# Performance work log

Measured on AMD Instinct MI355X. Metric: run time of the kernel, lower is better.

Reference implementation:

```python
import jax, jax.numpy as jnp
import numpy as np

E, R, K, D, B = 100000, 1000, 200, 256, 65536  # entities, relations, bundle heads, emb dim, batch


def setup_inputs() -> dict:
    key = jax.random.key(0)
    ks = jax.random.split(key, 12)
    ent_emb = jax.random.normal(ks[0], (E, D), dtype=jnp.float32)
    ent_emb = ent_emb / jnp.linalg.norm(ent_emb, axis=1, keepdims=True)  # xavier + L2 row-normalize
    heads = jax.random.normal(ks[1], (K, D), dtype=jnp.float32)
    heads = heads / jnp.linalg.norm(heads, axis=1, keepdims=True)  # normalize_vvrel_embeddings
    bases = jax.random.normal(ks[2], (R, 2, D), dtype=jnp.float32)
    bases = bases / jnp.linalg.norm(bases, axis=2, keepdims=True)  # normalize_all_rows
    rel2head = jax.random.randint(ks[3], (R,), 0, K)              # r_id2_vrr[rel][0] -> head idx
    rel2mult = jnp.where(jax.random.bernoulli(ks[4], 0.5, (R,)), 1.0, -1.0).astype(jnp.float32)  # r_id2_vrr[rel][1]
    return {
        'pos_h': jax.random.randint(ks[5], (B,), 0, E),
        'pos_t': jax.random.randint(ks[6], (B,), 0, E),
        'pos_r': jax.random.randint(ks[7], (B,), 0, R),
        'neg_h': jax.random.randint(ks[8], (B,), 0, E),
        'neg_t': jax.random.randint(ks[9], (B,), 0, E),
        'neg_r': jax.random.randint(ks[10], (B,), 0, R),
        'ent_emb': ent_emb, 'heads': heads, 'bases': bases,
        'rel2head': rel2head, 'rel2mult': rel2mult,
    }


def _transint_scores(pos_h, pos_t, pos_r, neg_h, neg_t, ent_emb, heads, bases, rel2head, rel2mult):
    # vvrel_embedding_func: head embedding scaled by +-1 multiplier
    r_e = heads[rel2head[pos_r]] * rel2mult[pos_r][:, None]           # [B, D]
    pos_sub = ent_emb[pos_h] + r_e - ent_emb[pos_t]                    # [B, D]
    neg_sub = ent_emb[neg_h] + r_e - ent_emb[neg_t]                    # [B, D] (note: uses pos_r_e, as in source)
    sub = jnp.concatenate([pos_sub, neg_sub], axis=0)                  # [2B, D]
    A = bases[jnp.concatenate([pos_r, pos_r], axis=0)]                 # [2B, 2, D] per-sample basis (comb_mats gather)
    # ATA and closed-form 2x2 inverse (module's `inverse`)
    ATA = jnp.einsum('bkd,bld->bkl', A, A)                             # [2B, 2, 2]
    a, b = ATA[:, 0, 0], ATA[:, 0, 1]
    c, d = ATA[:, 1, 0], ATA[:, 1, 1]
    det = a * d - b * c
    safe_det = jnp.where(det != 0, det, 1.0)
    inv_reg = jnp.stack([jnp.stack([d, -b], -1), jnp.stack([-c, a], -1)], -2) / safe_det[:, None, None]
    inv_fb = jnp.eye(2, dtype=ATA.dtype)[None] / a[:, None, None]      # fallback when det == 0
    ATA_inv = jnp.where((det != 0)[:, None, None], inv_reg, inv_fb)    # [2B, 2, 2]
    # P @ sub with P = I - A^T (A A^T)^{-1} A, applied without materializing P
    Asub = jnp.einsum('bkd,bd->bk', A, sub)                            # [2B, 2]
    proj = sub - jnp.einsum('bkd,bk->bd', A, jnp.einsum('bkl,bl->bk', ATA_inv, Asub))
    score = jnp.sum(proj ** 2, axis=1)                                 # L1_flag = False -> squared L2
    nb = pos_h.shape[0]
    return score[:nb], score[nb:]


def reference(pos_h, pos_t, pos_r, neg_h, neg_t, neg_r, ent_emb, heads, bases, rel2head, rel2mult):
    return _transint_scores(pos_h, pos_t, pos_r, neg_h, neg_t, ent_emb, heads, bases, rel2head, rel2mult)
```

## Files before the change

kernel.cpp:

```cpp
#include <hip/hip_runtime.h>

#define D 256
#define D4 (D/4)

__device__ inline float dot4(const float4 u, const float4 v) {
    return u.x*v.x + u.y*v.y + u.z*v.z + u.w*v.w;
}

__device__ inline float wsum(float v) {
    #pragma unroll
    for (int off = 32; off > 0; off >>= 1)
        v += __shfl_xor(v, off, 64);
    return v;
}

__global__ __launch_bounds__(256) void transint_pre(
    const float* __restrict__ heads,
    const float* __restrict__ bases,
    const int*   __restrict__ rel2head,
    const float* __restrict__ rel2mult,
    float*       __restrict__ re_buf,
    float*       __restrict__ par_buf,
    int R)
{
    const int wave = (blockIdx.x * blockDim.x + threadIdx.x) >> 6;
    const int lane = threadIdx.x & 63;
    if (wave >= R) return;
    const int r = wave;

    const int hd = rel2head[r];
    const float mult = rel2mult[r];
    const float4* hrow = (const float4*)(heads + (size_t)hd * D);
    const float4* arow = (const float4*)(bases + (size_t)r * 2 * D);

    float4 a0 = arow[lane];
    float4 a1 = arow[D4 + lane];
    float4 re = hrow[lane];
    re.x *= mult; re.y *= mult; re.z *= mult; re.w *= mult;
    ((float4*)(re_buf + (size_t)r * D))[lane] = re;

    float aa = wsum(dot4(a0, a0));
    float ab = wsum(dot4(a0, a1));
    float dd = wsum(dot4(a1, a1));

    float det = aa * dd - ab * ab;
    float m00, m01, m11;
    if (det != 0.0f) {
        float inv = 1.0f / det;
        m00 = dd * inv; m01 = -ab * inv; m11 = aa * inv;
    } else {
        float inv = 1.0f / aa;
        m00 = inv; m01 = 0.0f; m11 = inv;
    }
    if (lane == 0) {
        float* p = par_buf + (size_t)r * 8;
        p[0] = m00; p[1] = m01; p[2] = m11;
        p[3] = aa;  p[4] = ab;  p[5] = dd;
        p[6] = 0.0f; p[7] = 0.0f;
    }
}

__global__ __launch_bounds__(256) void transint_main(
    const int*   __restrict__ pos_h,
    const int*   __restrict__ pos_t,
    const int*   __restrict__ pos_r,
    const int*   __restrict__ neg_h,
    const int*   __restrict__ neg_t,
    const float* __restrict__ ent_emb,
    const float* __restrict__ bases,
    const float* __restrict__ re_buf,
    const float* __restrict__ par_buf,
    float*       __restrict__ out,
    int nB)
{
    const int wave = (blockIdx.x * blockDim.x + threadIdx.x) >> 6;
    const int lane = threadIdx.x & 63;
    const int g    = lane >> 4;
    const int gl   = lane & 15;
    const int b    = wave * 4 + g;
    if (b >= nB) return;

    const int r  = pos_r[b];
    const int ph = pos_h[b];
    const int pt = pos_t[b];
    const int nh = neg_h[b];
    const int nt = neg_t[b];

    const float4* e   = (const float4*)ent_emb;
    const float4* a0p = (const float4*)(bases + (size_t)r * 2 * D);
    const float4* a1p = a0p + D4;
    const float4* rep = (const float4*)(re_buf + (size_t)r * D);
    const float4* php = e + (size_t)ph * D4;
    const float4* ptp = e + (size_t)pt * D4;
    const float4* nhp = e + (size_t)nh * D4;
    const float4* ntp = e + (size_t)nt * D4;

    float p0 = 0.f, p1 = 0.f, n0 = 0.f, n1 = 0.f, ssp = 0.f, ssn = 0.f;

    #pragma unroll
    for (int c = 0; c < 4; ++c) {
        const int idx = gl + 16 * c;
        float4 a0 = a0p[idx];
        float4 a1 = a1p[idx];
        float4 re = rep[idx];
        float4 eh = php[idx];
        float4 et = ptp[idx];
        float4 xh = nhp[idx];
        float4 xt = ntp[idx];

        float4 ps, ns;
        ps.x = eh.x + re.x - et.x;  ns.x = xh.x + re.x - xt.x;
        ps.y = eh.y + re.y - et.y;  ns.y = xh.y + re.y - xt.y;
        ps.z = eh.z + re.z - et.z;  ns.z = xh.z + re.z - xt.z;
        ps.w = eh.w + re.w - et.w;  ns.w = xh.w + re.w - xt.w;

        p0  += dot4(a0, ps);
        p1  += dot4(a1, ps);
        n0  += dot4(a0, ns);
        n1  += dot4(a1, ns);
        ssp += dot4(ps, ps);
        ssn += dot4(ns, ns);
    }

    #pragma unroll
    for (int off = 8; off > 0; off >>= 1) {
        p0  += __shfl_xor(p0,  off, 64);
        p1  += __shfl_xor(p1,  off, 64);
        n0  += __shfl_xor(n0,  off, 64);
        n1  += __shfl_xor(n1,  off, 64);
        ssp += __shfl_xor(ssp, off, 64);
        ssn += __shfl_xor(ssn, off, 64);
    }

    const float* par = par_buf + (size_t)r * 8;
    const float m00 = par[0], m01 = par[1], m11 = par[2];
    const float aa  = par[3], ab  = par[4], dd  = par[5];

    float c0 = m00 * p0 + m01 * p1;
    float c1 = m01 * p0 + m11 * p1;
    float sp = ssp - 2.f * (p0 * c0 + p1 * c1)
             + (aa * c0 * c0 + 2.f * ab * c0 * c1 + dd * c1 * c1);

    float d0 = m00 * n0 + m01 * n1;
    float d1 = m01 * n0 + m11 * n1;
    float sn = ssn - 2.f * (n0 * d0 + n1 * d1)
             + (aa * d0 * d0 + 2.f * ab * d0 * d1 + dd * d1 * d1);

    if (gl == 0) {
        out[b]      = sp;
        out[nB + b] = sn;
    }
}

extern "C" void kernel_launch(void* const* d_in, const int* in_sizes, int n_in,
                              void* d_out, int out_size, void* d_ws, size_t ws_size,
                              hipStream_t stream) {
    const int*   pos_h    = (const int*)  d_in[0];
    const int*   pos_t    = (const int*)  d_in[1];
    const int*   pos_r    = (const int*)  d_in[2];
    const int*   neg_h    = (const int*)  d_in[3];
    const int*   neg_t    = (const int*)  d_in[4];
    const float* ent_emb  = (const float*)d_in[6];
    const float* heads    = (const float*)d_in[7];
    const float* bases    = (const float*)d_in[8];
    const int*   rel2head = (const int*)  d_in[9];
    const float* rel2mult = (const float*)d_in[10];
    float* out = (float*)d_out;

    const int nB = in_sizes[0];
    const int R  = in_sizes[9];

    float* re_buf  = (float*)d_ws;
    float* par_buf = re_buf + (size_t)R * D;

    {
        const int waves_per_block = 4;
        dim3 grid((R + waves_per_block - 1) / waves_per_block);
        transint_pre<<<grid, dim3(256), 0, stream>>>(
            heads, bases, rel2head, rel2mult, re_buf, par_buf, R);
    }

    {
        const int samples_per_block = 16;
        dim3 grid((nB + samples_per_block - 1) / samples_per_block);
        transint_main<<<grid, dim3(256), 0, stream>>>(
            pos_h, pos_t, pos_r, neg_h, neg_t,
            ent_emb, bases, re_buf, par_buf, out, nB);
    }
}
```

Before: 195.2 us.

## Convert entity table to fp16 per call and gather half-precision rows

Adds a pre-pass kernel that converts the whole entity embedding table to packed fp16 in workspace on every call. The main kernel then gathers half-width rows and unpacks them to fp32 for the projection math. The goal is to halve the bytes moved by the four random row gathers per sample. In exchange, each call pays a full-table read plus a half-size write, and the scores lose precision from fp16 rounding. The fp32 path is kept as a fallback when the workspace is too small.

```diff
diff --git a/kernel.cpp b/kernel.cpp
--- a/kernel.cpp
+++ b/kernel.cpp
@@ -2,6 +2,9 @@
 
 #define D 256
 #define D4 (D/4)
+#define D8 (D/8)
+
+typedef __fp16 f16x2 __attribute__((ext_vector_type(2)));
 
 __device__ inline float dot4(const float4 u, const float4 v) {
     return u.x*v.x + u.y*v.y + u.z*v.z + u.w*v.w;
@@ -12,6 +15,41 @@
     for (int off = 32; off > 0; off >>= 1)
         v += __shfl_xor(v, off, 64);
     return v;
+}
+
+__device__ inline unsigned pack2(float a, float b) {
+    f16x2 h = __builtin_amdgcn_cvt_pkrtz(a, b);
+    return *(unsigned*)&h;
+}
+
+__device__ inline void unpack2(unsigned u, float& a, float& b) {
+    f16x2 h = *(f16x2*)&u;
+    a = (float)h.x;
+    b = (float)h.y;
+}
+
+__device__ inline void unpack8(const int4 v, float* f) {
+    const unsigned* u = (const unsigned*)&v;
+    #pragma unroll
+    for (int i = 0; i < 4; ++i)
+        unpack2(u[i], f[2*i], f[2*i+1]);
+}
+
+__global__ __launch_bounds__(256) void transint_conv(
+    const float4* __restrict__ src, int4* __restrict__ dst, int n)
+{
+    int stride = gridDim.x * blockDim.x;
+    for (int i = blockIdx.x * blockDim.x + threadIdx.x; i < n; i += stride) {
+        float4 x = src[2*i];
+        float4 y = src[2*i+1];
+        int4 o;
+        unsigned* u = (unsigned*)&o;
+        u[0] = pack2(x.x, x.y);
+        u[1] = pack2(x.z, x.w);
+        u[2] = pack2(y.x, y.y);
+        u[3] = pack2(y.z, y.w);
+        dst[i] = o;
+    }
 }
 
 __global__ __launch_bounds__(256) void transint_pre(
@@ -60,7 +98,105 @@
     }
 }
 
-__global__ __launch_bounds__(256) void transint_main(
+__global__ __launch_bounds__(256) void transint_main_h(
+    const int*   __restrict__ pos_h,
+    const int*   __restrict__ pos_t,
+    const int*   __restrict__ pos_r,
+    const int*   __restrict__ neg_h,
+    const int*   __restrict__ neg_t,
+    const int4*  __restrict__ ent_h,
+    const float* __restrict__ bases,
+    const float* __restrict__ re_buf,
+    const float* __restrict__ par_buf,
+    float*       __restrict__ out,
+    int nB)
+{
+    const int wave = (blockIdx.x * blockDim.x + threadIdx.x) >> 6;
+    const int lane = threadIdx.x & 63;
+    const int g    = lane >> 4;
+    const int gl   = lane & 15;
+    const int b    = wave * 4 + g;
+    if (b >= nB) return;
+
+    const int r  = pos_r[b];
+    const int ph = pos_h[b];
+    const int pt = pos_t[b];
+    const int nh = neg_h[b];
+    const int nt = neg_t[b];
+
+    const int4* php = ent_h + (size_t)ph * D8;
+    const int4* ptp = ent_h + (size_t)pt * D8;
+    const int4* nhp = ent_h + (size_t)nh * D8;
+    const int4* ntp = ent_h + (size_t)nt * D8;
+    const float4* a0p = (const float4*)(bases + (size_t)r * 2 * D);
+    const float4* a1p = a0p + D4;
+    const float4* rep = (const float4*)(re_buf + (size_t)r * D);
+
+    float p0 = 0.f, p1 = 0.f, n0 = 0.f, n1 = 0.f, ssp = 0.f, ssn = 0.f;
+
+    #pragma unroll
+    for (int c = 0; c < 2; ++c) {
+        const int idx = gl + 16 * c;
+        int4 rh = php[idx];
+        int4 rt = ptp[idx];
+        int4 qh = nhp[idx];
+        int4 qt = ntp[idx];
+        float4 a0a = a0p[2*idx],   a0b = a0p[2*idx+1];
+        float4 a1a = a1p[2*idx],   a1b = a1p[2*idx+1];
+        float4 rea = rep[2*idx],   reb = rep[2*idx+1];
+
+        float eh[8], et[8], xh[8], xt[8];
+        unpack8(rh, eh); unpack8(rt, et);
+        unpack8(qh, xh); unpack8(qt, xt);
+
+        float a0f[8] = {a0a.x,a0a.y,a0a.z,a0a.w, a0b.x,a0b.y,a0b.z,a0b.w};
+        float a1f[8] = {a1a.x,a1a.y,a1a.z,a1a.w, a1b.x,a1b.y,a1b.z,a1b.w};
+        float ref[8] = {rea.x,rea.y,rea.z,rea.w, reb.x,reb.y,reb.z,reb.w};
+
+        #pragma unroll
+        for (int j = 0; j < 8; ++j) {
+            float ps = eh[j] + ref[j] - et[j];
+            float ns = xh[j] + ref[j] - xt[j];
+            p0  += a0f[j] * ps;
+            p1  += a1f[j] * ps;
+            n0  += a0f[j] * ns;
+            n1  += a1f[j] * ns;
+            ssp += ps * ps;
+            ssn += ns * ns;
+        }
+    }
+
+    #pragma unroll
+    for (int off = 8; off > 0; off >>= 1) {
+        p0  += __shfl_xor(p0,  off, 64);
+        p1  += __shfl_xor(p1,  off, 64);
+        n0  += __shfl_xor(n0,  off, 64);
+        n1  += __shfl_xor(n1,  off, 64);
+        ssp += __shfl_xor(ssp, off, 64);
+        ssn += __shfl_xor(ssn, off, 64);
+    }
+
+    const float* par = par_buf + (size_t)r * 8;
+    const float m00 = par[0], m01 = par[1], m11 = par[2];
+    const float aa  = par[3], ab  = par[4], dd  = par[5];
+
+    float c0 = m00 * p0 + m01 * p1;
+    float c1 = m01 * p0 + m11 * p1;
+    float sp = ssp - 2.f * (p0 * c0 + p1 * c1)
+             + (aa * c0 * c0 + 2.f * ab * c0 * c1 + dd * c1 * c1);
+
+    float d0 = m00 * n0 + m01 * n1;
+    float d1 = m01 * n0 + m11 * n1;
+    float sn = ssn - 2.f * (n0 * d0 + n1 * d1)
+             + (aa * d0 * d0 + 2.f * ab * d0 * d1 + dd * d1 * d1);
+
+    if (gl == 0) {
+        out[b]      = sp;
+        out[nB + b] = sn;
+    }
+}
+
+__global__ __launch_bounds__(256) void transint_main_f(
     const int*   __restrict__ pos_h,
     const int*   __restrict__ pos_t,
     const int*   __restrict__ pos_r,
@@ -169,22 +305,48 @@
 
     const int nB = in_sizes[0];
     const int R  = in_sizes[9];
-
-    float* re_buf  = (float*)d_ws;
-    float* par_buf = re_buf + (size_t)R * D;
-
-    {
-        const int waves_per_block = 4;
-        dim3 grid((R + waves_per_block - 1) / waves_per_block);
-        transint_pre<<<grid, dim3(256), 0, stream>>>(
-            heads, bases, rel2head, rel2mult, re_buf, par_buf, R);
-    }
-
-    {
-        const int samples_per_block = 16;
-        dim3 grid((nB + samples_per_block - 1) / samples_per_block);
-        transint_main<<<grid, dim3(256), 0, stream>>>(
-            pos_h, pos_t, pos_r, neg_h, neg_t,
-            ent_emb, bases, re_buf, par_buf, out, nB);
-    }
-}
+    const int E  = in_sizes[6] / D;
+
+    const size_t ent_half_bytes = (size_t)E * D * 2;
+    const size_t re_bytes       = (size_t)R * D * 4;
+    const size_t par_bytes      = (size_t)R * 8 * 4;
+    const bool use_fp16 = ws_size >= ent_half_bytes + re_bytes + par_bytes;
+
+    if (use_fp16) {
+        int4*  ent_h   = (int4*)d_ws;
+        float* re_buf  = (float*)((char*)d_ws + ent_half_bytes);
+        float* par_buf = re_buf + (size_t)R * D;
+
+        {
+            dim3 grid((R + 3) / 4);
+            transint_pre<<<grid, dim3(256), 0, stream>>>(
+                heads, bases, rel2head, rel2mult, re_buf, par_buf, R);
+        }
+        {
+            int n = E * D / 8;
+            int blocks = 4096;
+            transint_conv<<<dim3(blocks), dim3(256), 0, stream>>>(
+                (const float4*)ent_emb, (int4*)ent_h, n);
+        }
+        {
+            dim3 grid((nB + 15) / 16);
+            transint_main_h<<<grid, dim3(256), 0, stream>>>(
+                pos_h, pos_t, pos_r, neg_h, neg_t,
+                ent_h, bases, re_buf, par_buf, out, nB);
+        }
+    } else {
+        float* re_buf  = (float*)d_ws;
+        float* par_buf = re_buf + (size_t)R * D;
+        {
+            dim3 grid((R + 3) / 4);
+            transint_pre<<<grid, dim3(256), 0, stream>>>(
+                heads, bases, rel2head, rel2mult, re_buf, par_buf, R);
+        }
+        {
+            dim3 grid((nB + 15) / 16);
+            transint_main_f<<<grid, dim3(256), 0, stream>>>(
+                pos_h, pos_t, pos_r, neg_h, neg_t,
+                ent_emb, bases, re_buf, par_buf, out, nB);
+        }
+    }
+}
```

Result: slower. 214.5 us (+9.9%).

## Store orthonormalized relation basis and translation in fp16 with folded quadratic form

Applied to the files above, without the earlier changes.

The pre-pass now orthonormalizes each relation's two basis rows with Gram-Schmidt and folds the 2x2 inverse into a single symmetric matrix. It packs the orthonormal basis and the relation translation vector into fp16, so per-sample relation reads are halved and the final correction is one quadratic form. The main kernel also reads entity rows as 8-element chunks, two float4 loads per step. Entity gathers, which make up most of the traffic, stay fp32, so the relation reads this saves are mostly served from cache. The fp16 rounding of the basis and translation adds numerical error.

```diff
diff --git a/kernel.cpp b/kernel.cpp
--- a/kernel.cpp
+++ b/kernel.cpp
@@ -2,6 +2,10 @@
 
 #define D 256
 #define D4 (D/4)
+#define D16 (D/8)
+#define RELW (3*(D/2))
+
+typedef __fp16 f16x2 __attribute__((ext_vector_type(2)));
 
 __device__ inline float dot4(const float4 u, const float4 v) {
     return u.x*v.x + u.y*v.y + u.z*v.z + u.w*v.w;
@@ -12,6 +16,24 @@
     for (int off = 32; off > 0; off >>= 1)
         v += __shfl_xor(v, off, 64);
     return v;
+}
+
+__device__ inline unsigned pack2(float a, float b) {
+    f16x2 h = __builtin_amdgcn_cvt_pkrtz(a, b);
+    return *(unsigned*)&h;
+}
+
+__device__ inline void unpack2(unsigned u, float& a, float& b) {
+    f16x2 h = *(f16x2*)&u;
+    a = (float)h.x;
+    b = (float)h.y;
+}
+
+__device__ inline void unpack8(const int4 v, float* f) {
+    const unsigned* u = (const unsigned*)&v;
+    #pragma unroll
+    for (int i = 0; i < 4; ++i)
+        unpack2(u[i], f[2*i], f[2*i+1]);
 }
 
 __global__ __launch_bounds__(256) void transint_pre(
@@ -19,7 +41,7 @@
     const float* __restrict__ bases,
     const int*   __restrict__ rel2head,
     const float* __restrict__ rel2mult,
-    float*       __restrict__ re_buf,
+    unsigned*    __restrict__ rel_h,
     float*       __restrict__ par_buf,
     int R)
 {
@@ -37,7 +59,6 @@
     float4 a1 = arow[D4 + lane];
     float4 re = hrow[lane];
     re.x *= mult; re.y *= mult; re.z *= mult; re.w *= mult;
-    ((float4*)(re_buf + (size_t)r * D))[lane] = re;
 
     float aa = wsum(dot4(a0, a0));
     float ab = wsum(dot4(a0, a1));
@@ -52,11 +73,44 @@
         float inv = 1.0f / aa;
         m00 = inv; m01 = 0.0f; m11 = inv;
     }
+    float t00 = aa * m00 + ab * m01;
+    float t01 = aa * m01 + ab * m11;
+    float t10 = ab * m00 + dd * m01;
+    float t11 = ab * m01 + dd * m11;
+    float q00 = 2.f * m00 - (m00 * t00 + m01 * t10);
+    float q01 = 2.f * m01 - (m00 * t01 + m01 * t11);
+    float q11 = 2.f * m11 - (m01 * t01 + m11 * t11);
+
+    float c00 = sqrtf(aa);
+    float ic00 = (c00 > 0.f) ? 1.f / c00 : 0.f;
+    float4 u0;
+    u0.x = a0.x * ic00; u0.y = a0.y * ic00; u0.z = a0.z * ic00; u0.w = a0.w * ic00;
+    float c10 = ab * ic00;
+    float4 v;
+    v.x = a1.x - c10 * u0.x; v.y = a1.y - c10 * u0.y;
+    v.z = a1.z - c10 * u0.z; v.w = a1.w - c10 * u0.w;
+    float vv = wsum(dot4(v, v));
+    float c11 = sqrtf(vv);
+    float ic11 = (c11 > 0.f) ? 1.f / c11 : 0.f;
+    float4 u1;
+    u1.x = v.x * ic11; u1.y = v.y * ic11; u1.z = v.z * ic11; u1.w = v.w * ic11;
+
+    float s00 = c00*c00*q00 + 2.f*c00*c10*q01 + c10*c10*q11;
+    float s01 = c00*c11*q01 + c10*c11*q11;
+    float s11 = c11*c11*q11;
+
+    unsigned* base = rel_h + (size_t)r * RELW;
+    uint2 w;
+    w.x = pack2(u0.x, u0.y); w.y = pack2(u0.z, u0.w);
+    ((uint2*)(base))[lane] = w;
+    w.x = pack2(u1.x, u1.y); w.y = pack2(u1.z, u1.w);
+    ((uint2*)(base + 128))[lane] = w;
+    w.x = pack2(re.x, re.y); w.y = pack2(re.z, re.w);
+    ((uint2*)(base + 256))[lane] = w;
+
     if (lane == 0) {
-        float* p = par_buf + (size_t)r * 8;
-        p[0] = m00; p[1] = m01; p[2] = m11;
-        p[3] = aa;  p[4] = ab;  p[5] = dd;
-        p[6] = 0.0f; p[7] = 0.0f;
+        float* p = par_buf + (size_t)r * 4;
+        p[0] = s00; p[1] = s01; p[2] = s11; p[3] = 0.f;
     }
 }
 
@@ -67,8 +121,7 @@
     const int*   __restrict__ neg_h,
     const int*   __restrict__ neg_t,
     const float* __restrict__ ent_emb,
-    const float* __restrict__ bases,
-    const float* __restrict__ re_buf,
+    const unsigned* __restrict__ rel_h,
     const float* __restrict__ par_buf,
     float*       __restrict__ out,
     int nB)
@@ -87,64 +140,64 @@
     const int nt = neg_t[b];
 
     const float4* e   = (const float4*)ent_emb;
-    const float4* a0p = (const float4*)(bases + (size_t)r * 2 * D);
-    const float4* a1p = a0p + D4;
-    const float4* rep = (const float4*)(re_buf + (size_t)r * D);
     const float4* php = e + (size_t)ph * D4;
     const float4* ptp = e + (size_t)pt * D4;
     const float4* nhp = e + (size_t)nh * D4;
     const float4* ntp = e + (size_t)nt * D4;
-
-    float p0 = 0.f, p1 = 0.f, n0 = 0.f, n1 = 0.f, ssp = 0.f, ssn = 0.f;
-
-    #pragma unroll
-    for (int c = 0; c < 4; ++c) {
-        const int idx = gl + 16 * c;
-        float4 a0 = a0p[idx];
-        float4 a1 = a1p[idx];
-        float4 re = rep[idx];
-        float4 eh = php[idx];
-        float4 et = ptp[idx];
-        float4 xh = nhp[idx];
-        float4 xt = ntp[idx];
-
-        float4 ps, ns;
-        ps.x = eh.x + re.x - et.x;  ns.x = xh.x + re.x - xt.x;
-        ps.y = eh.y + re.y - et.y;  ns.y = xh.y + re.y - xt.y;
-        ps.z = eh.z + re.z - et.z;  ns.z = xh.z + re.z - xt.z;
-        ps.w = eh.w + re.w - et.w;  ns.w = xh.w + re.w - xt.w;
-
-        p0  += dot4(a0, ps);
-        p1  += dot4(a1, ps);
-        n0  += dot4(a0, ns);
-        n1  += dot4(a1, ns);
-        ssp += dot4(ps, ps);
-        ssn += dot4(ns, ns);
+    const unsigned* rb = rel_h + (size_t)r * RELW;
+    const int4* u0p = (const int4*)rb;
+    const int4* u1p = (const int4*)(rb + 128);
+    const int4* rep = (const int4*)(rb + 256);
+
+    float pp0 = 0.f, pp1 = 0.f, pn0 = 0.f, pn1 = 0.f, ssp = 0.f, ssn = 0.f;
+
+    #pragma unroll
+    for (int c = 0; c < 2; ++c) {
+        const int idx8 = gl + 16 * c;
+        int4 u0c = u0p[idx8];
+        int4 u1c = u1p[idx8];
+        int4 rec = rep[idx8];
+        float4 eh0 = php[2*idx8], eh1 = php[2*idx8+1];
+        float4 et0 = ptp[2*idx8], et1 = ptp[2*idx8+1];
+        float4 xh0 = nhp[2*idx8], xh1 = nhp[2*idx8+1];
+        float4 xt0 = ntp[2*idx8], xt1 = ntp[2*idx8+1];
+
+        float u0f[8], u1f[8], ref[8];
+        unpack8(u0c, u0f); unpack8(u1c, u1f); unpack8(rec, ref);
+
+        float ehf[8] = {eh0.x,eh0.y,eh0.z,eh0.w, eh1.x,eh1.y,eh1.z,eh1.w};
+        float etf[8] = {et0.x,et0.y,et0.z,et0.w, et1.x,et1.y,et1.z,et1.w};
+        float xhf[8] = {xh0.x,xh0.y,xh0.z,xh0.w, xh1.x,xh1.y,xh1.z,xh1.w};
+        float xtf[8] = {xt0.x,xt0.y,xt0.z,xt0.w, xt1.x,xt1.y,xt1.z,xt1.w};
+
+        #pragma unroll
+        for (int j = 0; j < 8; ++j) {
+            float ps = ehf[j] + ref[j] - etf[j];
+            float ns = xhf[j] + ref[j] - xtf[j];
+            pp0 += u0f[j] * ps;
+            pp1 += u1f[j] * ps;
+            pn0 += u0f[j] * ns;
+            pn1 += u1f[j] * ns;
+            ssp += ps * ps;
+            ssn += ns * ns;
+        }
     }
 
     #pragma unroll
     for (int off = 8; off > 0; off >>= 1) {
-        p0  += __shfl_xor(p0,  off, 64);
-        p1  += __shfl_xor(p1,  off, 64);
-        n0  += __shfl_xor(n0,  off, 64);
-        n1  += __shfl_xor(n1,  off, 64);
+        pp0 += __shfl_xor(pp0, off, 64);
+        pp1 += __shfl_xor(pp1, off, 64);
+        pn0 += __shfl_xor(pn0, off, 64);
+        pn1 += __shfl_xor(pn1, off, 64);
         ssp += __shfl_xor(ssp, off, 64);
         ssn += __shfl_xor(ssn, off, 64);
     }
 
-    const float* par = par_buf + (size_t)r * 8;
-    const float m00 = par[0], m01 = par[1], m11 = par[2];
-    const float aa  = par[3], ab  = par[4], dd  = par[5];
-
-    float c0 = m00 * p0 + m01 * p1;
-    float c1 = m01 * p0 + m11 * p1;
-    float sp = ssp - 2.f * (p0 * c0 + p1 * c1)
-             + (aa * c0 * c0 + 2.f * ab * c0 * c1 + dd * c1 * c1);
-
-    float d0 = m00 * n0 + m01 * n1;
-    float d1 = m01 * n0 + m11 * n1;
-    float sn = ssn - 2.f * (n0 * d0 + n1 * d1)
-             + (aa * d0 * d0 + 2.f * ab * d0 * d1 + dd * d1 * d1);
+    const float* par = par_buf + (size_t)r * 4;
+    const float s00 = par[0], s01 = par[1], s11 = par[2];
+
+    float sp = ssp - (s00*pp0*pp0 + 2.f*s01*pp0*pp1 + s11*pp1*pp1);
+    float sn = ssn - (s00*pn0*pn0 + 2.f*s01*pn0*pn1 + s11*pn1*pn1);
 
     if (gl == 0) {
         out[b]      = sp;
@@ -170,21 +223,18 @@
     const int nB = in_sizes[0];
     const int R  = in_sizes[9];
 
-    float* re_buf  = (float*)d_ws;
-    float* par_buf = re_buf + (size_t)R * D;
+    unsigned* rel_h   = (unsigned*)d_ws;
+    float*    par_buf = (float*)(rel_h + (size_t)R * RELW);
 
     {
-        const int waves_per_block = 4;
-        dim3 grid((R + waves_per_block - 1) / waves_per_block);
+        dim3 grid((R + 3) / 4);
         transint_pre<<<grid, dim3(256), 0, stream>>>(
-            heads, bases, rel2head, rel2mult, re_buf, par_buf, R);
-    }
-
+            heads, bases, rel2head, rel2mult, rel_h, par_buf, R);
+    }
     {
-        const int samples_per_block = 16;
-        dim3 grid((nB + samples_per_block - 1) / samples_per_block);
+        dim3 grid((nB + 15) / 16);
         transint_main<<<grid, dim3(256), 0, stream>>>(
             pos_h, pos_t, pos_r, neg_h, neg_t,
-            ent_emb, bases, re_buf, par_buf, out, nB);
-    }
-}
+            ent_emb, rel_h, par_buf, out, nB);
+    }
+}
```

Result: no change. 193.3 us (-0.9%).
